# Optimization experiments

Measured on AMD Instinct MI355X. Metric: run time of the kernel, lower is better.

## Reference

```python
import jax, jax.numpy as jnp
import numpy as np

N_VARS = 4000
N_LITS = 2 * N_VARS
N_CLAUSES = 16000
N_CELLS = 48000
DIM = 128
N_ROUNDS = 16
N_PROBS = 8


def _mlp(x, w1, b1, w2, b2, w3, b3):
    x = jax.nn.relu(x @ w1.T + b1)
    x = jax.nn.relu(x @ w2.T + b2)
    return x @ w3.T + b3


def _lstm_step(x, h, c, wih, whh, bih, bhh):
    # PyTorch LSTM gate order: i, f, g, o
    gates = x @ wih.T + bih + h @ whh.T + bhh
    i, f, g, o = jnp.split(gates, 4, axis=-1)
    c = jax.nn.sigmoid(f) * c + jax.nn.sigmoid(i) * jnp.tanh(g)
    h = jax.nn.sigmoid(o) * jnp.tanh(c)
    return h, c


def setup_inputs() -> dict:
    key = jax.random.key(0)
    ks = iter(jax.random.split(key, 64))

    def p(shape, scale=0.05):
        return jax.random.normal(next(ks), shape, dtype=jnp.float32) * scale

    lit_idx = jax.random.randint(next(ks), (N_CELLS,), 0, N_LITS)
    cls_idx = jax.random.randint(next(ks), (N_CELLS,), 0, N_CLAUSES)
    L_unpack_indices = jnp.stack([lit_idx, cls_idx], axis=1)  # [n_cells, 2]

    return dict(
        L_unpack_indices=L_unpack_indices,
        n_vars=N_VARS, n_probs=N_PROBS, n_rounds=N_ROUNDS,
        L_init_w=p((DIM, 1)), L_init_b=p((DIM,)),
        C_init_w=p((DIM, 1)), C_init_b=p((DIM,)),
        Lmsg_w1=p((DIM, DIM)), Lmsg_b1=p((DIM,)),
        Lmsg_w2=p((DIM, DIM)), Lmsg_b2=p((DIM,)),
        Lmsg_w3=p((DIM, DIM)), Lmsg_b3=p((DIM,)),
        Cmsg_w1=p((DIM, DIM)), Cmsg_b1=p((DIM,)),
        Cmsg_w2=p((DIM, DIM)), Cmsg_b2=p((DIM,)),
        Cmsg_w3=p((DIM, DIM)), Cmsg_b3=p((DIM,)),
        Lvote_w1=p((DIM, DIM)), Lvote_b1=p((DIM,)),
        Lvote_w2=p((DIM, DIM)), Lvote_b2=p((DIM,)),
        Lvote_w3=p((1, DIM)), Lvote_b3=p((1,)),
        Lu_wih=p((4 * DIM, 2 * DIM)), Lu_whh=p((4 * DIM, DIM)),
        Lu_bih=p((4 * DIM,)), Lu_bhh=p((4 * DIM,)),
        Cu_wih=p((4 * DIM, DIM)), Cu_whh=p((4 * DIM, DIM)),
        Cu_bih=p((4 * DIM,)), Cu_bhh=p((4 * DIM,)),
    )


def reference(L_unpack_indices, n_vars, n_probs, n_rounds,
              L_init_w, L_init_b, C_init_w, C_init_b,
              Lmsg_w1, Lmsg_b1, Lmsg_w2, Lmsg_b2, Lmsg_w3, Lmsg_b3,
              Cmsg_w1, Cmsg_b1, Cmsg_w2, Cmsg_b2, Cmsg_w3, Cmsg_b3,
              Lvote_w1, Lvote_b1, Lvote_w2, Lvote_b2, Lvote_w3, Lvote_b3,
              Lu_wih, Lu_whh, Lu_bih, Lu_bhh,
              Cu_wih, Cu_whh, Cu_bih, Cu_bhh):
    n_lits = 2 * n_vars
    dim = L_init_b.shape[0]
    n_clauses = N_CLAUSES

    # densified literal-clause incidence matrix (matches torch.sparse -> to_dense)
    M = jnp.zeros((n_lits, n_clauses), jnp.float32).at[
        L_unpack_indices[:, 0], L_unpack_indices[:, 1]].add(1.0)

    # L_init/C_init applied to ts = ones(1)
    L0 = jnp.broadcast_to(L_init_w[:, 0] + L_init_b, (n_lits, dim))
    C0 = jnp.broadcast_to(C_init_w[:, 0] + C_init_b, (n_clauses, dim))
    carry0 = (L0, jnp.zeros((n_lits, dim), jnp.float32),
              C0, jnp.zeros((n_clauses, dim), jnp.float32))

    def round_fn(carry, _):
        Lh, Lc, Ch, Cc = carry
        L_pre = _mlp(Lh, Lmsg_w1, Lmsg_b1, Lmsg_w2, Lmsg_b2, Lmsg_w3, Lmsg_b3)
        LC_msg = M.T @ L_pre                      # [n_clauses, dim]
        Ch, Cc = _lstm_step(LC_msg, Ch, Cc, Cu_wih, Cu_whh, Cu_bih, Cu_bhh)
        C_pre = _mlp(Ch, Cmsg_w1, Cmsg_b1, Cmsg_w2, Cmsg_b2, Cmsg_w3, Cmsg_b3)
        CL_msg = M @ C_pre                        # [n_lits, dim]
        flipped = jnp.concatenate([Lh[n_vars:2 * n_vars], Lh[:n_vars]], axis=0)
        Lh, Lc = _lstm_step(jnp.concatenate([CL_msg, flipped], axis=1),
                            Lh, Lc, Lu_wih, Lu_whh, Lu_bih, Lu_bhh)
        return (Lh, Lc, Ch, Cc), None

    (Lh, _, _, _), _ = jax.lax.scan(round_fn, carry0, None, length=n_rounds)

    vote = _mlp(Lh, Lvote_w1, Lvote_b1, Lvote_w2, Lvote_b2, Lvote_w3, Lvote_b3)  # [n_lits, 1]
    vote_join = jnp.concatenate([vote[:n_vars], vote[n_vars:]], axis=1)          # [n_vars, 2]
    vote_join = vote_join.reshape(n_probs, -1)
    return jnp.mean(vote_join, axis=1)
```

## Files before the change

### kernel.cpp

```cpp
#include <hip/hip_runtime.h>
#include <cstdint>
#include <cstddef>

#define N_VARS   4000
#define N_LITS   8000
#define N_CLAUSES 16000
#define N_CELLS  48000
#define DIM      128
#define N_ROUNDS 16
#define N_PROBS  8

typedef __bf16 bf16x8 __attribute__((ext_vector_type(8)));
typedef float f32x4 __attribute__((ext_vector_type(4)));

__device__ inline unsigned short f2bf(float x) {
  unsigned int u = __float_as_uint(x);
  u += 0x7fffu + ((u >> 16) & 1u);
  return (unsigned short)(u >> 16);
}
__device__ inline float bflo(unsigned int v) { return __uint_as_float(v << 16); }
__device__ inline float bfhi(unsigned int v) { return __uint_as_float(v & 0xffff0000u); }
__device__ inline unsigned int pack2(float a, float b) {
  return (unsigned int)f2bf(a) | ((unsigned int)f2bf(b) << 16);
}
__device__ inline bf16x8 ld_frag(const unsigned short* p) {
  uint4 u = *reinterpret_cast<const uint4*>(p);
  return __builtin_bit_cast(bf16x8, u);
}
__device__ inline float fast_sigmoid(float x) { return 1.f / (1.f + __expf(-x)); }
__device__ inline float fast_tanh(float x) {
  float t = __expf(-2.f * x);
  return (1.f - t) / (1.f + t);
}


template<int KS, int RG, bool LIT>
__global__ __launch_bounds__(512, 4) void fused_round(
    const int* __restrict__ ptr, const int* __restrict__ col,
    const unsigned short* __restrict__ Tsrc,
    const unsigned short* hold, unsigned short* hnew,
    float* __restrict__ cst,
    const unsigned short* __restrict__ Wp, const float* __restrict__ bP,
    const unsigned short* __restrict__ Wm1, const float* __restrict__ bm1,
    const unsigned short* __restrict__ Wm2, const float* __restrict__ bm2,
    const unsigned short* __restrict__ Wm3, const float* __restrict__ bm3,
    unsigned short* __restrict__ Tout) {
  constexpr int ROWS = RG * 16;
  __shared__ __align__(16) unsigned short msg[ROWS][136];
  __shared__ __align__(16) unsigned short hsA[ROWS][136];
  __shared__ __align__(16) unsigned short hsF[LIT ? ROWS : 1][136];
  __shared__ __align__(16) unsigned short xb[ROWS][136];
  __shared__ __align__(16) unsigned short pmsg[RG == 1 ? 3 : 1][RG == 1 ? 16 : 1][136];
  const int tid = threadIdx.x;
  const int w = tid >> 6, l = tid & 63;
  const int r = l & 15, kc = l >> 4;
  const int row0 = blockIdx.x * ROWS;

  uint4 stA[2], stF[2];
  if (tid >= 256) {
    const int sidx = tid - 256;
#pragma unroll
    for (int q = 0; q < RG; ++q) {
      const int n = sidx + q * 256;
      const int rw = n >> 4, c8 = (n & 15) * 8;
      stA[q] = *reinterpret_cast<const uint4*>(&hold[(size_t)(row0 + rw) * 128 + c8]);
      if (LIT) {
        const int gr = row0 + rw;
        const int fr = (gr < N_VARS) ? gr + N_VARS : gr - N_VARS;
        stF[q] = *reinterpret_cast<const uint4*>(&hold[(size_t)fr * 128 + c8]);
      }
    }
  }

  float s[16];
  {
    const int g8 = tid >> 3, gl = tid & 7;
    const int grow = (RG == 2) ? (g8 & 31) : (g8 & 15);
    const int part = (RG == 2) ? (g8 >> 5) : (g8 >> 4);
    constexpr int NPART = (RG == 2) ? 2 : 4;
    const int row = row0 + grow;
    const int b = ptr[row], e = ptr[row + 1];
#pragma unroll
    for (int q = 0; q < 16; ++q) s[q] = 0.f;
    int j = b + part;
    int c0 = (j < e) ? col[j] : 0;
    while (j < e) {
      const int jn = j + NPART;
      const int c1 = (jn < e) ? col[jn] : 0;
      const unsigned short* src = &Tsrc[(size_t)c0 * 128 + gl * 16];
      const uint4 v0 = *reinterpret_cast<const uint4*>(src);
      const uint4 v1 = *reinterpret_cast<const uint4*>(src + 8);
      s[0]  += bflo(v0.x); s[1]  += bfhi(v0.x);
      s[2]  += bflo(v0.y); s[3]  += bfhi(v0.y);
      s[4]  += bflo(v0.z); s[5]  += bfhi(v0.z);
      s[6]  += bflo(v0.w); s[7]  += bfhi(v0.w);
      s[8]  += bflo(v1.x); s[9]  += bfhi(v1.x);
      s[10] += bflo(v1.y); s[11] += bfhi(v1.y);
      s[12] += bflo(v1.z); s[13] += bfhi(v1.z);
      s[14] += bflo(v1.w); s[15] += bfhi(v1.w);
      j = jn; c0 = c1;
    }
    if (part > 0) {
      uint4 o0, o1;
      o0.x = pack2(s[0], s[1]);  o0.y = pack2(s[2], s[3]);
      o0.z = pack2(s[4], s[5]);  o0.w = pack2(s[6], s[7]);
      o1.x = pack2(s[8], s[9]);  o1.y = pack2(s[10], s[11]);
      o1.z = pack2(s[12], s[13]); o1.w = pack2(s[14], s[15]);
      unsigned short* dst = (RG == 2) ? &msg[grow][gl * 16]
                                      : &pmsg[part - 1][grow][gl * 16];
      *reinterpret_cast<uint4*>(dst) = o0;
      *reinterpret_cast<uint4*>(dst + 8) = o1;
    }
  }
  __syncthreads();

  {
    const int g8 = tid >> 3, gl = tid & 7;
    const int grow = (RG == 2) ? (g8 & 31) : (g8 & 15);
    const int part = (RG == 2) ? (g8 >> 5) : (g8 >> 4);
    if (part == 0) {
      if (RG == 2) {
        const uint4 m0 = *reinterpret_cast<const uint4*>(&msg[grow][gl * 16]);
        const uint4 m1 = *reinterpret_cast<const uint4*>(&msg[grow][gl * 16 + 8]);
        s[0]  += bflo(m0.x); s[1]  += bfhi(m0.x);
        s[2]  += bflo(m0.y); s[3]  += bfhi(m0.y);
        s[4]  += bflo(m0.z); s[5]  += bfhi(m0.z);
        s[6]  += bflo(m0.w); s[7]  += bfhi(m0.w);
        s[8]  += bflo(m1.x); s[9]  += bfhi(m1.x);
        s[10] += bflo(m1.y); s[11] += bfhi(m1.y);
        s[12] += bflo(m1.z); s[13] += bfhi(m1.z);
        s[14] += bflo(m1.w); s[15] += bfhi(m1.w);
      } else {
#pragma unroll
        for (int p = 0; p < 3; ++p) {
          const uint4 m0 = *reinterpret_cast<const uint4*>(&pmsg[p][grow][gl * 16]);
          const uint4 m1 = *reinterpret_cast<const uint4*>(&pmsg[p][grow][gl * 16 + 8]);
          s[0]  += bflo(m0.x); s[1]  += bfhi(m0.x);
          s[2]  += bflo(m0.y); s[3]  += bfhi(m0.y);
          s[4]  += bflo(m0.z); s[5]  += bfhi(m0.z);
          s[6]  += bflo(m0.w); s[7]  += bfhi(m0.w);
          s[8]  += bflo(m1.x); s[9]  += bfhi(m1.x);
          s[10] += bflo(m1.y); s[11] += bfhi(m1.y);
          s[12] += bflo(m1.z); s[13] += bfhi(m1.z);
          s[14] += bflo(m1.w); s[15] += bfhi(m1.w);
        }
      }
      uint4 o0, o1;
      o0.x = pack2(s[0], s[1]);  o0.y = pack2(s[2], s[3]);
      o0.z = pack2(s[4], s[5]);  o0.w = pack2(s[6], s[7]);
      o1.x = pack2(s[8], s[9]);  o1.y = pack2(s[10], s[11]);
      o1.z = pack2(s[12], s[13]); o1.w = pack2(s[14], s[15]);
      *reinterpret_cast<uint4*>(&msg[grow][gl * 16]) = o0;
      *reinterpret_cast<uint4*>(&msg[grow][gl * 16 + 8]) = o1;
    } else if (tid >= 256) {
      const int sidx = tid - 256;
#pragma unroll
      for (int q = 0; q < RG; ++q) {
        const int n = sidx + q * 256;
        const int rw = n >> 4, c8 = (n & 15) * 8;
        *reinterpret_cast<uint4*>(&hsA[rw][c8]) = stA[q];
        if (LIT)
          *reinterpret_cast<uint4*>(&hsF[rw][c8]) = stF[q];
      }
    }
  }
  __syncthreads();

  f32x4 acc[RG][4];
#pragma unroll
  for (int rg = 0; rg < RG; ++rg)
#pragma unroll
    for (int t = 0; t < 4; ++t) acc[rg][t] = (f32x4){0.f, 0.f, 0.f, 0.f};

#pragma unroll
  for (int ks = 0; ks < KS; ++ks) {
    bf16x8 bfr[RG];
#pragma unroll
    for (int rg = 0; rg < RG; ++rg) {
      const int xr = rg * 16 + r;
      if (ks < 4)        bfr[rg] = ld_frag(&msg[xr][ks * 32 + kc * 8]);
      else if (!LIT)     bfr[rg] = ld_frag(&hsA[xr][(ks - 4) * 32 + kc * 8]);
      else if (ks < 8)   bfr[rg] = ld_frag(&hsF[xr][(ks - 4) * 32 + kc * 8]);
      else               bfr[rg] = ld_frag(&hsA[xr][(ks - 8) * 32 + kc * 8]);
    }
#pragma unroll
    for (int tt = 0; tt < 4; ++tt) {
      bf16x8 afr = ld_frag(&Wp[(size_t)(((w * KS + ks) * 4 + tt) * 64 + l) * 8]);
#pragma unroll
      for (int rg = 0; rg < RG; ++rg)
        acc[rg][tt] = __builtin_amdgcn_mfma_f32_16x16x32_bf16(afr, bfr[rg], acc[rg][tt], 0, 0, 0);
    }
  }
  __syncthreads();

  {
    const int d0 = w * 16 + kc * 4;
#pragma unroll
    for (int rg = 0; rg < RG; ++rg) {
      const int row = row0 + rg * 16 + r;
      const size_t cb = (size_t)row * 128 + d0;
      f32x4 cv = *reinterpret_cast<const f32x4*>(&cst[cb]);
      f32x4 cn4;
      unsigned int hp[2];
#pragma unroll
      for (int tt = 0; tt < 4; ++tt) {
        const float4 bb = *reinterpret_cast<const float4*>(&bP[w * 64 + tt * 16 + kc * 4]);
        float ig = acc[rg][tt][0] + bb.x;
        float fg = acc[rg][tt][1] + bb.y;
        float gg = acc[rg][tt][2] + bb.z;
        float og = acc[rg][tt][3] + bb.w;
        float cn = fast_sigmoid(fg) * cv[tt] + fast_sigmoid(ig) * fast_tanh(gg);
        float hv = fast_sigmoid(og) * fast_tanh(cn);
        cn4[tt] = cn;
        if (tt & 1) hp[tt >> 1] |= (unsigned int)f2bf(hv) << 16;
        else        hp[tt >> 1]  = (unsigned int)f2bf(hv);
      }
      *reinterpret_cast<f32x4*>(&cst[cb]) = cn4;
      uint2 hv2 = {hp[0], hp[1]};
      *reinterpret_cast<uint2*>(&hnew[cb]) = hv2;
      *reinterpret_cast<uint2*>(&hsA[rg * 16 + r][d0]) = hv2;
    }
  }
  __syncthreads();

  constexpr int TPW = (RG == 2) ? 2 : 1;
  const int mrg = (RG == 2) ? (w >> 2) : 0;
  const int t0 = (RG == 2) ? ((w & 3) * 2) : w;
  {
    f32x4 a2[TPW];
#pragma unroll
    for (int q = 0; q < TPW; ++q) a2[q] = (f32x4){0.f, 0.f, 0.f, 0.f};
#pragma unroll
    for (int ks = 0; ks < 4; ++ks) {
      bf16x8 af = ld_frag(&hsA[mrg * 16 + r][ks * 32 + kc * 8]);
#pragma unroll
      for (int q = 0; q < TPW; ++q) {
        bf16x8 bf = ld_frag(&Wm1[(size_t)(((t0 + q) * 4 + ks) * 64 + l) * 8]);
        a2[q] = __builtin_amdgcn_mfma_f32_16x16x32_bf16(af, bf, a2[q], 0, 0, 0);
      }
    }
#pragma unroll
    for (int q = 0; q < TPW; ++q) {
      float bv = bm1[(t0 + q) * 16 + r];
#pragma unroll
      for (int j = 0; j < 4; ++j)
        xb[mrg * 16 + kc * 4 + j][(t0 + q) * 16 + r] = f2bf(fmaxf(a2[q][j] + bv, 0.f));
    }
  }
  __syncthreads();
  {
    f32x4 a2[TPW];
#pragma unroll
    for (int q = 0; q < TPW; ++q) a2[q] = (f32x4){0.f, 0.f, 0.f, 0.f};
#pragma unroll
    for (int ks = 0; ks < 4; ++ks) {
      bf16x8 af = ld_frag(&xb[mrg * 16 + r][ks * 32 + kc * 8]);
#pragma unroll
      for (int q = 0; q < TPW; ++q) {
        bf16x8 bf = ld_frag(&Wm2[(size_t)(((t0 + q) * 4 + ks) * 64 + l) * 8]);
        a2[q] = __builtin_amdgcn_mfma_f32_16x16x32_bf16(af, bf, a2[q], 0, 0, 0);
      }
    }
#pragma unroll
    for (int q = 0; q < TPW; ++q) {
      float bv = bm2[(t0 + q) * 16 + r];
#pragma unroll
      for (int j = 0; j < 4; ++j)
        msg[mrg * 16 + kc * 4 + j][(t0 + q) * 16 + r] = f2bf(fmaxf(a2[q][j] + bv, 0.f));
    }
  }
  __syncthreads();
  {
    f32x4 a2[TPW];
#pragma unroll
    for (int q = 0; q < TPW; ++q) a2[q] = (f32x4){0.f, 0.f, 0.f, 0.f};
#pragma unroll
    for (int ks = 0; ks < 4; ++ks) {
      bf16x8 af = ld_frag(&msg[mrg * 16 + r][ks * 32 + kc * 8]);
#pragma unroll
      for (int q = 0; q < TPW; ++q) {
        bf16x8 bf = ld_frag(&Wm3[(size_t)(((t0 + q) * 4 + ks) * 64 + l) * 8]);
        a2[q] = __builtin_amdgcn_mfma_f32_16x16x32_bf16(af, bf, a2[q], 0, 0, 0);
      }
    }
#pragma unroll
    for (int q = 0; q < TPW; ++q) {
      float bv = bm3[(t0 + q) * 16 + r];
#pragma unroll
      for (int j = 0; j < 4; ++j)
        Tout[(size_t)(row0 + mrg * 16 + kc * 4 + j) * 128 + (t0 + q) * 16 + r] =
            f2bf(a2[q][j] + bv);
    }
  }
}

__global__ __launch_bounds__(256) void fused_mlp3(
    const unsigned short* __restrict__ A,
    const unsigned short* __restrict__ W1, const float* __restrict__ b1,
    const unsigned short* __restrict__ W2, const float* __restrict__ b2,
    const unsigned short* __restrict__ W3, const float* __restrict__ b3,
    unsigned short* __restrict__ out) {
  __shared__ __align__(16) unsigned short xbuf[2][4][16][136];
  const int w = threadIdx.x >> 6, l = threadIdx.x & 63;
  const int r = l & 15, kc = l >> 4;
  const int row0 = blockIdx.x * 64 + w * 16;

  f32x4 acc[8];
#pragma unroll
  for (int t = 0; t < 8; ++t) acc[t] = (f32x4){0.f, 0.f, 0.f, 0.f};
#pragma unroll
  for (int ks = 0; ks < 4; ++ks) {
    bf16x8 a = ld_frag(&A[(size_t)(row0 + r) * 128 + ks * 32 + kc * 8]);
#pragma unroll
    for (int t = 0; t < 8; ++t) {
      bf16x8 b = ld_frag(&W1[(size_t)((t * 4 + ks) * 64 + l) * 8]);
      acc[t] = __builtin_amdgcn_mfma_f32_16x16x32_bf16(a, b, acc[t], 0, 0, 0);
    }
  }
#pragma unroll
  for (int t = 0; t < 8; ++t) {
    float bv = b1[t * 16 + r];
#pragma unroll
    for (int j = 0; j < 4; ++j)
      xbuf[0][w][kc * 4 + j][t * 16 + r] = f2bf(fmaxf(acc[t][j] + bv, 0.f));
  }
#pragma unroll
  for (int t = 0; t < 8; ++t) acc[t] = (f32x4){0.f, 0.f, 0.f, 0.f};
#pragma unroll
  for (int ks = 0; ks < 4; ++ks) {
    bf16x8 a = ld_frag(&xbuf[0][w][r][ks * 32 + kc * 8]);
#pragma unroll
    for (int t = 0; t < 8; ++t) {
      bf16x8 b = ld_frag(&W2[(size_t)((t * 4 + ks) * 64 + l) * 8]);
      acc[t] = __builtin_amdgcn_mfma_f32_16x16x32_bf16(a, b, acc[t], 0, 0, 0);
    }
  }
#pragma unroll
  for (int t = 0; t < 8; ++t) {
    float bv = b2[t * 16 + r];
#pragma unroll
    for (int j = 0; j < 4; ++j)
      xbuf[1][w][kc * 4 + j][t * 16 + r] = f2bf(fmaxf(acc[t][j] + bv, 0.f));
  }
#pragma unroll
  for (int t = 0; t < 8; ++t) acc[t] = (f32x4){0.f, 0.f, 0.f, 0.f};
#pragma unroll
  for (int ks = 0; ks < 4; ++ks) {
    bf16x8 a = ld_frag(&xbuf[1][w][r][ks * 32 + kc * 8]);
#pragma unroll
    for (int t = 0; t < 8; ++t) {
      bf16x8 b = ld_frag(&W3[(size_t)((t * 4 + ks) * 64 + l) * 8]);
      acc[t] = __builtin_amdgcn_mfma_f32_16x16x32_bf16(a, b, acc[t], 0, 0, 0);
    }
  }
#pragma unroll
  for (int t = 0; t < 8; ++t) {
    float bv = b3[t * 16 + r];
#pragma unroll
    for (int j = 0; j < 4; ++j)
      out[(size_t)(row0 + kc * 4 + j) * 128 + t * 16 + r] = f2bf(acc[t][j] + bv);
  }
}

__global__ __launch_bounds__(256) void fused_vote(
    const unsigned short* __restrict__ A,
    const unsigned short* __restrict__ W1, const float* __restrict__ b1,
    const unsigned short* __restrict__ W2, const float* __restrict__ b2,
    const float* __restrict__ w3, const float* __restrict__ b3,
    float* __restrict__ vote) {
  __shared__ __align__(16) unsigned short xbuf[4][16][136];
  const int w = threadIdx.x >> 6, l = threadIdx.x & 63;
  const int r = l & 15, kc = l >> 4;
  const int row0 = blockIdx.x * 64 + w * 16;

  f32x4 acc[8];
#pragma unroll
  for (int t = 0; t < 8; ++t) acc[t] = (f32x4){0.f, 0.f, 0.f, 0.f};
#pragma unroll
  for (int ks = 0; ks < 4; ++ks) {
    bf16x8 a = ld_frag(&A[(size_t)(row0 + r) * 128 + ks * 32 + kc * 8]);
#pragma unroll
    for (int t = 0; t < 8; ++t) {
      bf16x8 b = ld_frag(&W1[(size_t)((t * 4 + ks) * 64 + l) * 8]);
      acc[t] = __builtin_amdgcn_mfma_f32_16x16x32_bf16(a, b, acc[t], 0, 0, 0);
    }
  }
#pragma unroll
  for (int t = 0; t < 8; ++t) {
    float bv = b1[t * 16 + r];
#pragma unroll
    for (int j = 0; j < 4; ++j)
      xbuf[w][kc * 4 + j][t * 16 + r] = f2bf(fmaxf(acc[t][j] + bv, 0.f));
  }
#pragma unroll
  for (int t = 0; t < 8; ++t) acc[t] = (f32x4){0.f, 0.f, 0.f, 0.f};
#pragma unroll
  for (int ks = 0; ks < 4; ++ks) {
    bf16x8 a = ld_frag(&xbuf[w][r][ks * 32 + kc * 8]);
#pragma unroll
    for (int t = 0; t < 8; ++t) {
      bf16x8 b = ld_frag(&W2[(size_t)((t * 4 + ks) * 64 + l) * 8]);
      acc[t] = __builtin_amdgcn_mfma_f32_16x16x32_bf16(a, b, acc[t], 0, 0, 0);
    }
  }
  float vs[4] = {0.f, 0.f, 0.f, 0.f};
#pragma unroll
  for (int t = 0; t < 8; ++t) {
    float bv = b2[t * 16 + r], wv = w3[t * 16 + r];
#pragma unroll
    for (int j = 0; j < 4; ++j)
      vs[j] += fmaxf(acc[t][j] + bv, 0.f) * wv;
  }
#pragma unroll
  for (int off = 1; off < 16; off <<= 1) {
#pragma unroll
    for (int j = 0; j < 4; ++j) vs[j] += __shfl_xor(vs[j], off, 16);
  }
  if (r == 0) {
#pragma unroll
    for (int j = 0; j < 4; ++j) vote[row0 + kc * 4 + j] = vs[j] + b3[0];
  }
}

__global__ void init_state_kernel(const float* __restrict__ Lw, const float* __restrict__ Lb,
                                  const float* __restrict__ Cw, const float* __restrict__ Cb,
                                  unsigned short* __restrict__ Lh, float* __restrict__ Lc,
                                  unsigned short* __restrict__ Ch, float* __restrict__ Cc) {
  int idx = blockIdx.x * 256 + threadIdx.x;
  if (idx >= N_CLAUSES * DIM) return;
  int d = idx & 127;
  Ch[idx] = f2bf(Cw[d] + Cb[d]);
  Cc[idx] = 0.f;
  if (idx < N_LITS * DIM) {
    Lh[idx] = f2bf(Lw[d] + Lb[d]);
    Lc[idx] = 0.f;
  }
}

__global__ void pack8_kernel(const float* s0, const float* s1, const float* s2, const float* s3,
                             const float* s4, const float* s5, const float* s6, const float* s7,
                             unsigned short* d0, unsigned short* d1, unsigned short* d2,
                             unsigned short* d3, unsigned short* d4, unsigned short* d5,
                             unsigned short* d6, unsigned short* d7) {
  int i = blockIdx.x * 256 + threadIdx.x;
  const float* s; unsigned short* d;
  switch (blockIdx.y) {
    case 0: s = s0; d = d0; break;
    case 1: s = s1; d = d1; break;
    case 2: s = s2; d = d2; break;
    case 3: s = s3; d = d3; break;
    case 4: s = s4; d = d4; break;
    case 5: s = s5; d = d5; break;
    case 6: s = s6; d = d6; break;
    default: s = s7; d = d7; break;
  }
  int np = i >> 7, k = i & 127;
  int tt = np >> 4, r = np & 15;
  int ks = k >> 5, kcf = (k >> 3) & 3, e = k & 7;
  int dst = (((tt * 4 + ks) * 64) + kcf * 16 + r) * 8 + e;
  d[dst] = f2bf(s[i]);
}

template<int KIH>
__global__ void pack_gates_kernel(const float* __restrict__ wih, const float* __restrict__ whh,
                                  const float* __restrict__ bih, const float* __restrict__ bhh,
                                  unsigned short* __restrict__ Wp, float* __restrict__ bP) {
  constexpr int K = KIH + 128;
  constexpr int KS = K / 32;
  int idx = blockIdx.x * 256 + threadIdx.x;
  if (idx >= 512 * K) return;
  int np = idx / K, k = idx % K;
  int gt = np & 3;
  int d = ((np >> 6) << 4) + (((np >> 2) & 3) << 2) + ((np >> 4) & 3);
  int orig = gt * 128 + d;
  float v = (k < KIH) ? wih[(size_t)orig * KIH + k] : whh[(size_t)orig * 128 + (k - KIH)];
  int w = np >> 6, tt = (np >> 4) & 3, rr = np & 15;
  int ks = k >> 5, kcf = (k >> 3) & 3, e = k & 7;
  size_t dst = ((size_t)((w * KS + ks) * 4 + tt) * 64 + kcf * 16 + rr) * 8 + e;
  Wp[dst] = f2bf(v);
  if (k == 0) bP[np] = bih[orig] + bhh[orig];
}

__global__ void count_kernel(const int* __restrict__ uidx,
                             int* __restrict__ lit_cnt, int* __restrict__ cls_cnt) {
  int i = blockIdx.x * 256 + threadIdx.x;
  if (i < N_CELLS) {
    atomicAdd(&lit_cnt[uidx[2 * i]], 1);
    atomicAdd(&cls_cnt[uidx[2 * i + 1]], 1);
  }
}

__global__ void scan_kernel(const int* __restrict__ cnt, int* __restrict__ ptr, int n) {
  __shared__ int part[1024];
  __shared__ int total;
  int t = threadIdx.x;
  int chunk = (n + 1023) >> 10;
  int lo = t * chunk, hi = min(lo + chunk, n);
  int s = 0;
  for (int i = lo; i < hi; ++i) s += cnt[i];
  part[t] = s;
  __syncthreads();
  if (t == 0) {
    int acc = 0;
    for (int i = 0; i < 1024; ++i) { int v = part[i]; part[i] = acc; acc += v; }
    total = acc;
  }
  __syncthreads();
  int acc = part[t];
  for (int i = lo; i < hi; ++i) { ptr[i] = acc; acc += cnt[i]; }
  if (t == 0) ptr[n] = total;
}

__global__ void scatter_kernel(const int* __restrict__ uidx,
                               const int* __restrict__ lit_ptr, const int* __restrict__ cls_ptr,
                               int* __restrict__ lit_fill, int* __restrict__ cls_fill,
                               int* __restrict__ lit_col, int* __restrict__ cls_col) {
  int i = blockIdx.x * 256 + threadIdx.x;
  if (i < N_CELLS) {
    int lit = uidx[2 * i], cls = uidx[2 * i + 1];
    int p = atomicAdd(&lit_fill[lit], 1);
    lit_col[lit_ptr[lit] + p] = cls;
    int q = atomicAdd(&cls_fill[cls], 1);
    cls_col[cls_ptr[cls] + q] = lit;
  }
}

__global__ void prob_mean_kernel(const float* __restrict__ vote, float* __restrict__ out) {
  int p = blockIdx.x;
  int t = threadIdx.x;
  float s = 0.f;
  for (int i = t; i < 500; i += 256) s += vote[p * 500 + i] + vote[N_VARS + p * 500 + i];
  __shared__ float red[256];
  red[t] = s;
  __syncthreads();
  for (int off = 128; off > 0; off >>= 1) {
    if (t < off) red[t] += red[t + off];
    __syncthreads();
  }
  if (t == 0) out[p] = red[0] * (1.0f / 1000.0f);
}

extern "C" void kernel_launch(void* const* d_in, const int* in_sizes, int n_in,
                              void* d_out, int out_size, void* d_ws, size_t ws_size,
                              hipStream_t stream) {
  (void)in_sizes; (void)n_in; (void)out_size;
  const int* uidx = (const int*)d_in[0];
  const float* L_init_w = (const float*)d_in[4];
  const float* L_init_b = (const float*)d_in[5];
  const float* C_init_w = (const float*)d_in[6];
  const float* C_init_b = (const float*)d_in[7];
  const float* Lmsg_w1 = (const float*)d_in[8],  *Lmsg_b1 = (const float*)d_in[9];
  const float* Lmsg_w2 = (const float*)d_in[10], *Lmsg_b2 = (const float*)d_in[11];
  const float* Lmsg_w3 = (const float*)d_in[12], *Lmsg_b3 = (const float*)d_in[13];
  const float* Cmsg_w1 = (const float*)d_in[14], *Cmsg_b1 = (const float*)d_in[15];
  const float* Cmsg_w2 = (const float*)d_in[16], *Cmsg_b2 = (const float*)d_in[17];
  const float* Cmsg_w3 = (const float*)d_in[18], *Cmsg_b3 = (const float*)d_in[19];
  const float* Lvote_w1 = (const float*)d_in[20], *Lvote_b1 = (const float*)d_in[21];
  const float* Lvote_w2 = (const float*)d_in[22], *Lvote_b2 = (const float*)d_in[23];
  const float* Lvote_w3 = (const float*)d_in[24], *Lvote_b3 = (const float*)d_in[25];
  const float* Lu_wih = (const float*)d_in[26], *Lu_whh = (const float*)d_in[27];
  const float* Lu_bih = (const float*)d_in[28], *Lu_bhh = (const float*)d_in[29];
  const float* Cu_wih = (const float*)d_in[30], *Cu_whh = (const float*)d_in[31];
  const float* Cu_bih = (const float*)d_in[32], *Cu_bhh = (const float*)d_in[33];
  float* out = (float*)d_out;

  char* base = (char*)d_ws;
  size_t off = 0;
  auto alloc = [&](size_t bytes) {
    void* p = base + off;
    off = (off + bytes + 255) & ~(size_t)255;
    return p;
  };
  float* Lc   = (float*)alloc((size_t)N_LITS * DIM * 4);
  float* Cc   = (float*)alloc((size_t)N_CLAUSES * DIM * 4);
  float* bL   = (float*)alloc(512 * 4);
  float* bC   = (float*)alloc(512 * 4);
  float* vote = (float*)alloc(N_LITS * 4);
  unsigned short* LhA = (unsigned short*)alloc((size_t)N_LITS * DIM * 2);
  unsigned short* LhB = (unsigned short*)alloc((size_t)N_LITS * DIM * 2);
  unsigned short* Ch  = (unsigned short*)alloc((size_t)N_CLAUSES * DIM * 2);
  unsigned short* TL  = (unsigned short*)alloc((size_t)N_LITS * DIM * 2);
  unsigned short* TC  = (unsigned short*)alloc((size_t)N_CLAUSES * DIM * 2);
  unsigned short* WLp = (unsigned short*)alloc(512 * 384 * 2);
  unsigned short* WCp = (unsigned short*)alloc(512 * 256 * 2);
  unsigned short* wLm1 = (unsigned short*)alloc(DIM * DIM * 2);
  unsigned short* wLm2 = (unsigned short*)alloc(DIM * DIM * 2);
  unsigned short* wLm3 = (unsigned short*)alloc(DIM * DIM * 2);
  unsigned short* wCm1 = (unsigned short*)alloc(DIM * DIM * 2);
  unsigned short* wCm2 = (unsigned short*)alloc(DIM * DIM * 2);
  unsigned short* wCm3 = (unsigned short*)alloc(DIM * DIM * 2);
  unsigned short* wV1  = (unsigned short*)alloc(DIM * DIM * 2);
  unsigned short* wV2  = (unsigned short*)alloc(DIM * DIM * 2);
  int* lit_cnt  = (int*)alloc(N_LITS * 4);
  int* cls_cnt  = (int*)alloc(N_CLAUSES * 4);
  int* lit_fill = (int*)alloc(N_LITS * 4);
  int* cls_fill = (int*)alloc(N_CLAUSES * 4);
  int* lit_ptr  = (int*)alloc((N_LITS + 1) * 4);
  int* cls_ptr  = (int*)alloc((N_CLAUSES + 1) * 4);
  int* lit_col  = (int*)alloc(N_CELLS * 4);
  int* cls_col  = (int*)alloc(N_CELLS * 4);
  if (off > ws_size) return;

  hipMemsetAsync(lit_cnt, 0, (char*)lit_ptr - (char*)lit_cnt, stream);
  count_kernel<<<(N_CELLS + 255) / 256, 256, 0, stream>>>(uidx, lit_cnt, cls_cnt);
  scan_kernel<<<1, 1024, 0, stream>>>(lit_cnt, lit_ptr, N_LITS);
  scan_kernel<<<1, 1024, 0, stream>>>(cls_cnt, cls_ptr, N_CLAUSES);
  scatter_kernel<<<(N_CELLS + 255) / 256, 256, 0, stream>>>(
      uidx, lit_ptr, cls_ptr, lit_fill, cls_fill, lit_col, cls_col);

  init_state_kernel<<<(N_CLAUSES * DIM + 255) / 256, 256, 0, stream>>>(
      L_init_w, L_init_b, C_init_w, C_init_b, LhA, Lc, Ch, Cc);
  pack_gates_kernel<256><<<(512 * 384 + 255) / 256, 256, 0, stream>>>(
      Lu_wih, Lu_whh, Lu_bih, Lu_bhh, WLp, bL);
  pack_gates_kernel<128><<<(512 * 256 + 255) / 256, 256, 0, stream>>>(
      Cu_wih, Cu_whh, Cu_bih, Cu_bhh, WCp, bC);
  dim3 cgrid(DIM * DIM / 256, 8);
  pack8_kernel<<<cgrid, 256, 0, stream>>>(
      Lmsg_w1, Lmsg_w2, Lmsg_w3, Cmsg_w1, Cmsg_w2, Cmsg_w3, Lvote_w1, Lvote_w2,
      wLm1, wLm2, wLm3, wCm1, wCm2, wCm3, wV1, wV2);

  fused_mlp3<<<N_LITS / 64, 256, 0, stream>>>(
      LhA, wLm1, Lmsg_b1, wLm2, Lmsg_b2, wLm3, Lmsg_b3, TL);

  for (int r = 0; r < N_ROUNDS; ++r) {
    fused_round<8, 2, false><<<N_CLAUSES / 32, 512, 0, stream>>>(
        cls_ptr, cls_col, TL, Ch, Ch, Cc, WCp, bC,
        wCm1, Cmsg_b1, wCm2, Cmsg_b2, wCm3, Cmsg_b3, TC);
    const unsigned short* lold = (r & 1) ? LhB : LhA;
    unsigned short* lnew = (r & 1) ? LhA : LhB;
    fused_round<12, 1, true><<<N_LITS / 16, 512, 0, stream>>>(
        lit_ptr, lit_col, TC, lold, lnew, Lc, WLp, bL,
        wLm1, Lmsg_b1, wLm2, Lmsg_b2, wLm3, Lmsg_b3, TL);
  }

  fused_vote<<<N_LITS / 64, 256, 0, stream>>>(
      LhA, wV1, Lvote_b1, wV2, Lvote_b2, Lvote_w3, Lvote_b3, vote);
  prob_mean_kernel<<<N_PROBS, 256, 0, stream>>>(vote, out);
}
```

Baseline: 715.4 us.

## Store LSTM cell state in bf16 and restructure MLP wave tiling

Cell state buffers for literals and clauses change from fp32 to bf16, which halves the read and write traffic for the per-round cell-state load and store. The fused MLP stages are also reorganised so each wave owns one 16-column output tile across all row groups, loading each weight fragment once and reusing it for every row group. An extra barrier is added before msg is written, because msg is still being read as a source earlier. Storing the cell state in bf16 across 16 recurrent rounds adds rounding error that can compound.

```diff
diff --git a/kernel.cpp b/kernel.cpp
--- a/kernel.cpp
+++ b/kernel.cpp
@@ -18,6 +18,9 @@
   u += 0x7fffu + ((u >> 16) & 1u);
   return (unsigned short)(u >> 16);
 }
+__device__ inline float bf2f(unsigned short v) {
+  return __uint_as_float((unsigned int)v << 16);
+}
 __device__ inline float bflo(unsigned int v) { return __uint_as_float(v << 16); }
 __device__ inline float bfhi(unsigned int v) { return __uint_as_float(v & 0xffff0000u); }
 __device__ inline unsigned int pack2(float a, float b) {
@@ -39,7 +42,7 @@
     const int* __restrict__ ptr, const int* __restrict__ col,
     const unsigned short* __restrict__ Tsrc,
     const unsigned short* hold, unsigned short* hnew,
-    float* __restrict__ cst,
+    unsigned short* __restrict__ cst,
     const unsigned short* __restrict__ Wp, const float* __restrict__ bP,
     const unsigned short* __restrict__ Wm1, const float* __restrict__ bm1,
     const unsigned short* __restrict__ Wm2, const float* __restrict__ bm2,
@@ -199,9 +202,9 @@
     for (int rg = 0; rg < RG; ++rg) {
       const int row = row0 + rg * 16 + r;
       const size_t cb = (size_t)row * 128 + d0;
-      f32x4 cv = *reinterpret_cast<const f32x4*>(&cst[cb]);
-      f32x4 cn4;
-      unsigned int hp[2];
+      const uint2 cv2 = *reinterpret_cast<const uint2*>(&cst[cb]);
+      const float cpv[4] = {bflo(cv2.x), bfhi(cv2.x), bflo(cv2.y), bfhi(cv2.y)};
+      unsigned int cp2[2], hp[2];
 #pragma unroll
       for (int tt = 0; tt < 4; ++tt) {
         const float4 bb = *reinterpret_cast<const float4*>(&bP[w * 64 + tt * 16 + kc * 4]);
@@ -209,13 +212,15 @@
         float fg = acc[rg][tt][1] + bb.y;
         float gg = acc[rg][tt][2] + bb.z;
         float og = acc[rg][tt][3] + bb.w;
-        float cn = fast_sigmoid(fg) * cv[tt] + fast_sigmoid(ig) * fast_tanh(gg);
+        float cn = fast_sigmoid(fg) * cpv[tt] + fast_sigmoid(ig) * fast_tanh(gg);
         float hv = fast_sigmoid(og) * fast_tanh(cn);
-        cn4[tt] = cn;
-        if (tt & 1) hp[tt >> 1] |= (unsigned int)f2bf(hv) << 16;
-        else        hp[tt >> 1]  = (unsigned int)f2bf(hv);
+        if (tt & 1) { cp2[tt >> 1] |= (unsigned int)f2bf(cn) << 16;
+                      hp[tt >> 1]  |= (unsigned int)f2bf(hv) << 16; }
+        else        { cp2[tt >> 1]  = (unsigned int)f2bf(cn);
+                      hp[tt >> 1]   = (unsigned int)f2bf(hv); }
       }
-      *reinterpret_cast<f32x4*>(&cst[cb]) = cn4;
+      uint2 cw = {cp2[0], cp2[1]};
+      *reinterpret_cast<uint2*>(&cst[cb]) = cw;
       uint2 hv2 = {hp[0], hp[1]};
       *reinterpret_cast<uint2*>(&hnew[cb]) = hv2;
       *reinterpret_cast<uint2*>(&hsA[rg * 16 + r][d0]) = hv2;
@@ -223,74 +228,69 @@
   }
   __syncthreads();
 
-  constexpr int TPW = (RG == 2) ? 2 : 1;
-  const int mrg = (RG == 2) ? (w >> 2) : 0;
-  const int t0 = (RG == 2) ? ((w & 3) * 2) : w;
   {
-    f32x4 a2[TPW];
-#pragma unroll
-    for (int q = 0; q < TPW; ++q) a2[q] = (f32x4){0.f, 0.f, 0.f, 0.f};
+    f32x4 a2[RG];
+#pragma unroll
+    for (int rg = 0; rg < RG; ++rg) a2[rg] = (f32x4){0.f, 0.f, 0.f, 0.f};
 #pragma unroll
     for (int ks = 0; ks < 4; ++ks) {
-      bf16x8 af = ld_frag(&hsA[mrg * 16 + r][ks * 32 + kc * 8]);
-#pragma unroll
-      for (int q = 0; q < TPW; ++q) {
-        bf16x8 bf = ld_frag(&Wm1[(size_t)(((t0 + q) * 4 + ks) * 64 + l) * 8]);
-        a2[q] = __builtin_amdgcn_mfma_f32_16x16x32_bf16(af, bf, a2[q], 0, 0, 0);
+      bf16x8 bf = ld_frag(&Wm1[(size_t)((w * 4 + ks) * 64 + l) * 8]);
+#pragma unroll
+      for (int rg = 0; rg < RG; ++rg) {
+        bf16x8 af = ld_frag(&hsA[rg * 16 + r][ks * 32 + kc * 8]);
+        a2[rg] = __builtin_amdgcn_mfma_f32_16x16x32_bf16(af, bf, a2[rg], 0, 0, 0);
       }
     }
-#pragma unroll
-    for (int q = 0; q < TPW; ++q) {
-      float bv = bm1[(t0 + q) * 16 + r];
+    float bv = bm1[w * 16 + r];
+#pragma unroll
+    for (int rg = 0; rg < RG; ++rg)
 #pragma unroll
       for (int j = 0; j < 4; ++j)
-        xb[mrg * 16 + kc * 4 + j][(t0 + q) * 16 + r] = f2bf(fmaxf(a2[q][j] + bv, 0.f));
-    }
+        xb[rg * 16 + kc * 4 + j][w * 16 + r] = f2bf(fmaxf(a2[rg][j] + bv, 0.f));
   }
   __syncthreads();
   {
-    f32x4 a2[TPW];
-#pragma unroll
-    for (int q = 0; q < TPW; ++q) a2[q] = (f32x4){0.f, 0.f, 0.f, 0.f};
+    f32x4 a2[RG];
+#pragma unroll
+    for (int rg = 0; rg < RG; ++rg) a2[rg] = (f32x4){0.f, 0.f, 0.f, 0.f};
 #pragma unroll
     for (int ks = 0; ks < 4; ++ks) {
-      bf16x8 af = ld_frag(&xb[mrg * 16 + r][ks * 32 + kc * 8]);
-#pragma unroll
-      for (int q = 0; q < TPW; ++q) {
-        bf16x8 bf = ld_frag(&Wm2[(size_t)(((t0 + q) * 4 + ks) * 64 + l) * 8]);
-        a2[q] = __builtin_amdgcn_mfma_f32_16x16x32_bf16(af, bf, a2[q], 0, 0, 0);
+      bf16x8 bf = ld_frag(&Wm2[(size_t)((w * 4 + ks) * 64 + l) * 8]);
+#pragma unroll
+      for (int rg = 0; rg < RG; ++rg) {
+        bf16x8 af = ld_frag(&xb[rg * 16 + r][ks * 32 + kc * 8]);
+        a2[rg] = __builtin_amdgcn_mfma_f32_16x16x32_bf16(af, bf, a2[rg], 0, 0, 0);
       }
     }
-#pragma unroll
-    for (int q = 0; q < TPW; ++q) {
-      float bv = bm2[(t0 + q) * 16 + r];
+    float bv = bm2[w * 16 + r];
+    __syncthreads();
+#pragma unroll
+    for (int rg = 0; rg < RG; ++rg)
 #pragma unroll
       for (int j = 0; j < 4; ++j)
-        msg[mrg * 16 + kc * 4 + j][(t0 + q) * 16 + r] = f2bf(fmaxf(a2[q][j] + bv, 0.f));
-    }
+        msg[rg * 16 + kc * 4 + j][w * 16 + r] = f2bf(fmaxf(a2[rg][j] + bv, 0.f));
   }
   __syncthreads();
   {
-    f32x4 a2[TPW];
-#pragma unroll
-    for (int q = 0; q < TPW; ++q) a2[q] = (f32x4){0.f, 0.f, 0.f, 0.f};
+    f32x4 a2[RG];
+#pragma unroll
+    for (int rg = 0; rg < RG; ++rg) a2[rg] = (f32x4){0.f, 0.f, 0.f, 0.f};
 #pragma unroll
     for (int ks = 0; ks < 4; ++ks) {
-      bf16x8 af = ld_frag(&msg[mrg * 16 + r][ks * 32 + kc * 8]);
-#pragma unroll
-      for (int q = 0; q < TPW; ++q) {
-        bf16x8 bf = ld_frag(&Wm3[(size_t)(((t0 + q) * 4 + ks) * 64 + l) * 8]);
-        a2[q] = __builtin_amdgcn_mfma_f32_16x16x32_bf16(af, bf, a2[q], 0, 0, 0);
+      bf16x8 bf = ld_frag(&Wm3[(size_t)((w * 4 + ks) * 64 + l) * 8]);
+#pragma unroll
+      for (int rg = 0; rg < RG; ++rg) {
+        bf16x8 af = ld_frag(&msg[rg * 16 + r][ks * 32 + kc * 8]);
+        a2[rg] = __builtin_amdgcn_mfma_f32_16x16x32_bf16(af, bf, a2[rg], 0, 0, 0);
       }
     }
-#pragma unroll
-    for (int q = 0; q < TPW; ++q) {
-      float bv = bm3[(t0 + q) * 16 + r];
+    float bv = bm3[w * 16 + r];
+#pragma unroll
+    for (int rg = 0; rg < RG; ++rg)
 #pragma unroll
       for (int j = 0; j < 4; ++j)
-        Tout[(size_t)(row0 + mrg * 16 + kc * 4 + j) * 128 + (t0 + q) * 16 + r] =
-            f2bf(a2[q][j] + bv);
-    }
+        Tout[(size_t)(row0 + rg * 16 + kc * 4 + j) * 128 + w * 16 + r] =
+            f2bf(a2[rg][j] + bv);
   }
 }
 
@@ -424,16 +424,16 @@
 
 __global__ void init_state_kernel(const float* __restrict__ Lw, const float* __restrict__ Lb,
                                   const float* __restrict__ Cw, const float* __restrict__ Cb,
-                                  unsigned short* __restrict__ Lh, float* __restrict__ Lc,
-                                  unsigned short* __restrict__ Ch, float* __restrict__ Cc) {
+                                  unsigned short* __restrict__ Lh, unsigned short* __restrict__ Lc,
+                                  unsigned short* __restrict__ Ch, unsigned short* __restrict__ Cc) {
   int idx = blockIdx.x * 256 + threadIdx.x;
   if (idx >= N_CLAUSES * DIM) return;
   int d = idx & 127;
   Ch[idx] = f2bf(Cw[d] + Cb[d]);
-  Cc[idx] = 0.f;
+  Cc[idx] = 0;
   if (idx < N_LITS * DIM) {
     Lh[idx] = f2bf(Lw[d] + Lb[d]);
-    Lc[idx] = 0.f;
+    Lc[idx] = 0;
   }
 }
 
@@ -571,8 +571,8 @@
     off = (off + bytes + 255) & ~(size_t)255;
     return p;
   };
-  float* Lc   = (float*)alloc((size_t)N_LITS * DIM * 4);
-  float* Cc   = (float*)alloc((size_t)N_CLAUSES * DIM * 4);
+  unsigned short* Lc = (unsigned short*)alloc((size_t)N_LITS * DIM * 2);
+  unsigned short* Cc = (unsigned short*)alloc((size_t)N_CLAUSES * DIM * 2);
   float* bL   = (float*)alloc(512 * 4);
   float* bC   = (float*)alloc(512 * 4);
   float* vote = (float*)alloc(N_LITS * 4);
```

New measurement: 704.1 us. About the same (-1.6%).
